# Kernel tuning notes

Hardware: AMD Instinct MI355X
Metric: run time of the kernel (lower is better)

Reference implementation:

```python
import jax, jax.numpy as jnp
import numpy as np

D_MODEL = 1024
D = 256
B, T = 64, 512


def setup_inputs() -> dict:
    key = jax.random.key(0)
    ks = jax.random.split(key, 7)
    s = 1.0 / np.sqrt(D_MODEL)
    return {
        "x": jax.random.normal(ks[0], (B, T, D_MODEL), dtype=jnp.float32),
        "Wq": jax.random.uniform(ks[1], (D_MODEL, D), jnp.float32, -s, s),
        "bq": jax.random.uniform(ks[2], (D,), jnp.float32, -s, s),
        "Wk": jax.random.uniform(ks[3], (D_MODEL, D), jnp.float32, -s, s),
        "bk": jax.random.uniform(ks[4], (D,), jnp.float32, -s, s),
        "Wv": jax.random.uniform(ks[5], (D_MODEL, D), jnp.float32, -s, s),
        "bv": jax.random.uniform(ks[6], (D,), jnp.float32, -s, s),
    }


def reference(x, Wq, bq, Wk, bk, Wv, bv):
    # Linear projections: [B,T,d_model] -> [B,T,d]
    q = x @ Wq + bq
    k = x @ Wk + bk
    v = x @ Wv + bv
    Tq = x.shape[1]
    scale = k.shape[-1] ** (-0.5)
    # scores: [B,T,T]
    scores = jnp.einsum('bqd,bkd->bqk', q, k) * scale
    causal = jnp.tril(jnp.ones((Tq, Tq), dtype=bool))
    scores = jnp.where(causal, scores, -jnp.inf)
    weights = jax.nn.softmax(scores, axis=-1)
    out = jnp.einsum('bqk,bkd->bqd', weights, v)
    return out
```

## Files before the change

### kernel.cpp

```cpp
#include <hip/hip_runtime.h>
#include <hip/hip_bf16.h>

typedef __attribute__((ext_vector_type(8))) short short8;
typedef __attribute__((ext_vector_type(4))) float floatx4;
typedef __attribute__((ext_vector_type(16))) float floatx16;

#define GLOAD_LDS16(src, dst) \
  __builtin_amdgcn_global_load_lds((const __attribute__((address_space(1))) unsigned int*)(src), \
      (__attribute__((address_space(3))) unsigned int*)(dst), 16, 0, 0)

__device__ __forceinline__ short f2bf(float f) {
    __hip_bfloat16 h = __float2bfloat16(f);
    return *reinterpret_cast<short*>(&h);
}

__device__ __forceinline__ floatx4 mfma16(short8 a, short8 b, floatx4 c) {
    return __builtin_amdgcn_mfma_f32_16x16x32_bf16(a, b, c, 0, 0, 0);
}

__device__ __forceinline__ floatx16 mfma32(short8 a, short8 b, floatx16 c) {
    return __builtin_amdgcn_mfma_f32_32x32x16_bf16(a, b, c, 0, 0, 0);
}

__global__ __launch_bounds__(256) void wconv_kernel(const float* __restrict__ Wq,
                                                    const float* __restrict__ Wk,
                                                    const float* __restrict__ Wv,
                                                    __hip_bfloat16* __restrict__ WT) {
    int n = blockIdx.x;
    const float* W = (n < 256) ? Wq : (n < 512 ? Wk : Wv);
    int nl = n & 255;
    __hip_bfloat16* dst = WT + (size_t)n * 1024;
    for (int kk = threadIdx.x; kk < 1024; kk += 256)
        dst[kk] = __float2bfloat16(W[(size_t)kk * 256 + nl]);
}

__global__ __launch_bounds__(512) void proj_kernel(const float* __restrict__ x,
                                                   const __hip_bfloat16* __restrict__ WT,
                                                   const float* __restrict__ bq,
                                                   const float* __restrict__ bk,
                                                   const float* __restrict__ bv,
                                                   __hip_bfloat16* __restrict__ qo,
                                                   __hip_bfloat16* __restrict__ ko,
                                                   __hip_bfloat16* __restrict__ vo) {
    __shared__ __align__(16) float As[128 * 64];
    __shared__ __align__(16) __hip_bfloat16 Bs[768 * 64];
    char* AsB = (char*)As;
    char* BsB = (char*)Bs;

    const int tid = threadIdx.x;
    const int m0 = blockIdx.x * 128;
    const int wid = tid >> 6, lane = tid & 63;
    const int wm = wid >> 2, wn = wid & 3;
    const int l31 = lane & 31, lh = lane >> 5;

    floatx16 acc[2][6];
#pragma unroll
    for (int i = 0; i < 2; ++i)
#pragma unroll
        for (int j = 0; j < 6; ++j)
#pragma unroll
            for (int e = 0; e < 16; ++e) acc[i][j][e] = 0.f;

    for (int kt = 0; kt < 16; ++kt) {
#pragma unroll
        for (int s = 0; s < 4; ++s) {
            int o = s * 8192 + tid * 16;
            int row = o >> 8;
            int sb = (o & 255) ^ ((row & 7) << 4);
            const float* src = x + (size_t)(m0 + row) * 1024 + kt * 64 + (sb >> 2);
            GLOAD_LDS16(src, AsB + o);
        }
#pragma unroll
        for (int s = 0; s < 12; ++s) {
            int o = s * 8192 + tid * 16;
            int row = o >> 7;
            int so = (o & 127) ^ ((row & 7) << 4);
            const __hip_bfloat16* src = WT + (size_t)row * 1024 + kt * 64 + (so >> 1);
            GLOAD_LDS16(src, BsB + o);
        }
        __syncthreads();

#pragma unroll
        for (int ks = 0; ks < 4; ++ks) {
            short8 af[2];
#pragma unroll
            for (int mt = 0; mt < 2; ++mt) {
                int row = wm * 64 + mt * 32 + l31;
                int rb = row * 256, msk = (row & 7) << 4;
                int b0 = ks * 64 + lh * 32;
                floatx4 f0 = *(const floatx4*)(AsB + rb + (b0 ^ msk));
                floatx4 f1 = *(const floatx4*)(AsB + rb + ((b0 + 16) ^ msk));
                short8 h;
                h[0] = f2bf(f0[0]); h[1] = f2bf(f0[1]); h[2] = f2bf(f0[2]); h[3] = f2bf(f0[3]);
                h[4] = f2bf(f1[0]); h[5] = f2bf(f1[1]); h[6] = f2bf(f1[2]); h[7] = f2bf(f1[3]);
                af[mt] = h;
            }
#pragma unroll
            for (int nt = 0; nt < 6; ++nt) {
                int row = wn * 192 + nt * 32 + l31;
                int off = ks * 32 + lh * 16;
                short8 b8 = *(const short8*)(BsB + row * 128 + (off ^ ((row & 7) << 4)));
                acc[0][nt] = mfma32(af[0], b8, acc[0][nt]);
                acc[1][nt] = mfma32(af[1], b8, acc[1][nt]);
            }
        }
        __syncthreads();
    }

#pragma unroll
    for (int nt = 0; nt < 6; ++nt) {
        int g = wn * 192 + nt * 32 + l31;
        int mat = g >> 8;
        const float* bias = (mat == 0) ? bq : (mat == 1 ? bk : bv);
        __hip_bfloat16* ob = (mat == 0) ? qo : (mat == 1 ? ko : vo);
        float scale = (mat == 0) ? 0.09016844005556021f : 1.0f;
        int c = g & 255;
        float bval = bias[c];
#pragma unroll
        for (int mt = 0; mt < 2; ++mt) {
            int base_row = m0 + wm * 64 + mt * 32 + lh * 4;
#pragma unroll
            for (int reg = 0; reg < 16; ++reg) {
                int row = base_row + (reg & 3) + 8 * (reg >> 2);
                ob[(size_t)row * 256 + c] = __float2bfloat16((acc[mt][nt][reg] + bval) * scale);
            }
        }
    }
}

__global__ __launch_bounds__(256) void attn_kernel(const __hip_bfloat16* __restrict__ q,
                                                   const __hip_bfloat16* __restrict__ k,
                                                   const __hip_bfloat16* __restrict__ v,
                                                   float* __restrict__ out) {
    __shared__ __align__(16) __hip_bfloat16 Ks[64 * 256];
    __shared__ __align__(16) __hip_bfloat16 VTs[256 * 64];
    __shared__ __align__(16) __hip_bfloat16 Ps[4][16 * 64];
    char* KsB = (char*)Ks;
    char* VTB = (char*)VTs;

    const int tid = threadIdx.x;
    const int bid = blockIdx.x;
    const int wgid = (bid & 7) * 64 + (bid >> 3);
    const int qb = wgid & 7, b = wgid >> 3;
    const int wid = tid >> 6, lane = tid & 63;
    const int l15 = lane & 15, lg = lane >> 4;
    char* PsB = (char*)(&Ps[wid][0]);

    short8 qf[8];
    const __hip_bfloat16* qrow = q + ((size_t)(b * 512 + qb * 64 + wid * 16 + l15)) * 256;
#pragma unroll
    for (int ks = 0; ks < 8; ++ks) qf[ks] = *(const short8*)(qrow + ks * 32 + lg * 8);

    float m_[4], lsum[4];
    floatx4 o[16];
#pragma unroll
    for (int r = 0; r < 4; ++r) { m_[r] = -1e30f; lsum[r] = 0.f; }
#pragma unroll
    for (int dt = 0; dt < 16; ++dt) o[dt] = (floatx4){0.f, 0.f, 0.f, 0.f};

    const int vkv = lane;
    const int vd0 = wid * 8;

    for (int c = 0; c <= qb; ++c) {
        const size_t kvbase = (size_t)(b * 512 + c * 64) * 256;
#pragma unroll
        for (int s = 0; s < 8; ++s) {
            int o_ = s * 4096 + tid * 16;
            int row = o_ >> 9;
            int so = o_ ^ ((row & 7) << 4);
            const __hip_bfloat16* src = k + kvbase + (size_t)row * 256 + ((so & 511) >> 1);
            GLOAD_LDS16(src, KsB + o_);
        }
#pragma unroll
        for (int it = 0; it < 8; ++it) {
            int dbase = vd0 + it * 32;
            short8 vv = *(const short8*)(v + kvbase + (size_t)vkv * 256 + dbase);
#pragma unroll
            for (int j = 0; j < 8; ++j) {
                int d = dbase + j;
                int addr = (d * 128 + vkv * 2) ^ ((d & 7) << 4);
                *(short*)(VTB + addr) = vv[j];
            }
        }
        __syncthreads();

        floatx4 s4[4];
#pragma unroll
        for (int t = 0; t < 4; ++t) s4[t] = (floatx4){0.f, 0.f, 0.f, 0.f};
#pragma unroll
        for (int ks = 0; ks < 8; ++ks) {
#pragma unroll
            for (int t = 0; t < 4; ++t) {
                int kv = t * 16 + l15;
                short8 kf = *(const short8*)(KsB + kv * 512 + ((ks * 64 + lg * 16) ^ ((kv & 7) << 4)));
                s4[t] = mfma16(qf[ks], kf, s4[t]);
            }
        }
        if (c == qb) {
#pragma unroll
            for (int t = 0; t < 4; ++t) {
                int kvl = t * 16 + l15;
#pragma unroll
                for (int r = 0; r < 4; ++r)
                    if (kvl > wid * 16 + lg * 4 + r) s4[t][r] = -1e30f;
            }
        }
        float pm[4], alpha[4], rs[4];
#pragma unroll
        for (int r = 0; r < 4; ++r)
            pm[r] = fmaxf(fmaxf(s4[0][r], s4[1][r]), fmaxf(s4[2][r], s4[3][r]));
#pragma unroll
        for (int off = 1; off <= 8; off <<= 1)
#pragma unroll
            for (int r = 0; r < 4; ++r) pm[r] = fmaxf(pm[r], __shfl_xor(pm[r], off));
#pragma unroll
        for (int r = 0; r < 4; ++r) {
            float mn = fmaxf(m_[r], pm[r]);
            alpha[r] = exp2f(m_[r] - mn);
            m_[r] = mn;
        }
#pragma unroll
        for (int t = 0; t < 4; ++t)
#pragma unroll
            for (int r = 0; r < 4; ++r) s4[t][r] = exp2f(s4[t][r] - m_[r]);
#pragma unroll
        for (int r = 0; r < 4; ++r) rs[r] = s4[0][r] + s4[1][r] + s4[2][r] + s4[3][r];
#pragma unroll
        for (int off = 1; off <= 8; off <<= 1)
#pragma unroll
            for (int r = 0; r < 4; ++r) rs[r] += __shfl_xor(rs[r], off);
#pragma unroll
        for (int r = 0; r < 4; ++r) lsum[r] = lsum[r] * alpha[r] + rs[r];
#pragma unroll
        for (int dt = 0; dt < 16; ++dt) {
            o[dt][0] *= alpha[0]; o[dt][1] *= alpha[1];
            o[dt][2] *= alpha[2]; o[dt][3] *= alpha[3];
        }
#pragma unroll
        for (int t = 0; t < 4; ++t)
#pragma unroll
            for (int r = 0; r < 4; ++r) {
                int qq = lg * 4 + r;
                int addr = (qq * 128 + (t * 16 + l15) * 2) ^ ((qq & 7) << 4);
                *(short*)(PsB + addr) = f2bf(s4[t][r]);
            }
#pragma unroll
        for (int h = 0; h < 2; ++h) {
            short8 pa = *(const short8*)(PsB + l15 * 128 + ((h * 64 + lg * 16) ^ ((l15 & 7) << 4)));
#pragma unroll
            for (int dt = 0; dt < 16; ++dt) {
                int d = dt * 16 + l15;
                short8 vb = *(const short8*)(VTB + d * 128 + ((h * 64 + lg * 16) ^ ((d & 7) << 4)));
                o[dt] = mfma16(pa, vb, o[dt]);
            }
        }
        __syncthreads();
    }

    float inv[4];
#pragma unroll
    for (int r = 0; r < 4; ++r) inv[r] = 1.0f / lsum[r];
    size_t obase = ((size_t)(b * 512 + qb * 64 + wid * 16 + lg * 4)) * 256 + l15;
#pragma unroll
    for (int dt = 0; dt < 16; ++dt)
#pragma unroll
        for (int r = 0; r < 4; ++r)
            out[obase + (size_t)r * 256 + dt * 16] = o[dt][r] * inv[r];
}

extern "C" void kernel_launch(void* const* d_in, const int* in_sizes, int n_in,
                              void* d_out, int out_size, void* d_ws, size_t ws_size,
                              hipStream_t stream) {
    const float* x  = (const float*)d_in[0];
    const float* Wq = (const float*)d_in[1];
    const float* bq = (const float*)d_in[2];
    const float* Wk = (const float*)d_in[3];
    const float* bk = (const float*)d_in[4];
    const float* Wv = (const float*)d_in[5];
    const float* bv = (const float*)d_in[6];
    float* out = (float*)d_out;

    char* ws = (char*)d_ws;
    __hip_bfloat16* WT = (__hip_bfloat16*)ws;
    __hip_bfloat16* qo = (__hip_bfloat16*)(ws + (2u << 20));
    __hip_bfloat16* ko = qo + (size_t)32768 * 256;
    __hip_bfloat16* vo = ko + (size_t)32768 * 256;

    wconv_kernel<<<dim3(768), dim3(256), 0, stream>>>(Wq, Wk, Wv, WT);
    proj_kernel<<<dim3(256), dim3(512), 0, stream>>>(x, WT, bq, bk, bv, qo, ko, vo);
    attn_kernel<<<dim3(512), dim3(256), 0, stream>>>(qo, ko, vo, out);
}
```

Before: 155.0 us.

## Double-buffer projection GEMM loads and tile the weight transpose through LDS

The projection GEMM now uses two LDS buffers with a K-step of 32, so async global-to-LDS loads for step kt+2 are issued while step kt is being computed. It uses vmcnt waits, raw barriers and MFMA priority hints in place of the old load-sync-compute loop. The weight transpose kernel is rewritten to transpose 64x64 tiles through padded shared memory, which gives coalesced reads and writes. The prefetch past the last step is clamped to a redundant reload of step 31, and the hand-set vmcnt count has to match the number of loads issued per stage.

Measured after the change: 159.1 us. 2.6% more time.

```diff
diff --git a/kernel.cpp b/kernel.cpp
--- a/kernel.cpp
+++ b/kernel.cpp
@@ -26,12 +26,29 @@
                                                     const float* __restrict__ Wk,
                                                     const float* __restrict__ Wv,
                                                     __hip_bfloat16* __restrict__ WT) {
-    int n = blockIdx.x;
-    const float* W = (n < 256) ? Wq : (n < 512 ? Wk : Wv);
-    int nl = n & 255;
-    __hip_bfloat16* dst = WT + (size_t)n * 1024;
-    for (int kk = threadIdx.x; kk < 1024; kk += 256)
-        dst[kk] = __float2bfloat16(W[(size_t)kk * 256 + nl]);
+    __shared__ unsigned short lds[64][65];
+    const int bidx = blockIdx.x;
+    const int kt = bidx & 15;
+    const int ntile = bidx >> 4;
+    const int gn0 = ntile * 64;
+    const float* W = (gn0 < 256) ? Wq : (gn0 < 512 ? Wk : Wv);
+    const int nl0 = gn0 & 255;
+    const int k0 = kt * 64;
+    const int tr = threadIdx.x >> 6;
+    const int tc = threadIdx.x & 63;
+
+#pragma unroll
+    for (int it = 0; it < 16; ++it) {
+        int r = it * 4 + tr;
+        lds[r][tc] = (unsigned short)f2bf(W[(size_t)(k0 + r) * 256 + nl0 + tc]);
+    }
+    __syncthreads();
+#pragma unroll
+    for (int it = 0; it < 16; ++it) {
+        int nr = it * 4 + tr;
+        unsigned short u = lds[tc][nr];
+        WT[(size_t)(gn0 + nr) * 1024 + k0 + tc] = *reinterpret_cast<__hip_bfloat16*>(&u);
+    }
 }
 
 __global__ __launch_bounds__(512) void proj_kernel(const float* __restrict__ x,
@@ -42,10 +59,8 @@
                                                    __hip_bfloat16* __restrict__ qo,
                                                    __hip_bfloat16* __restrict__ ko,
                                                    __hip_bfloat16* __restrict__ vo) {
-    __shared__ __align__(16) float As[128 * 64];
-    __shared__ __align__(16) __hip_bfloat16 Bs[768 * 64];
-    char* AsB = (char*)As;
-    char* BsB = (char*)Bs;
+    __shared__ __align__(16) char Ab[2][16384];
+    __shared__ __align__(16) char Bb[2][49152];
 
     const int tid = threadIdx.x;
     const int m0 = blockIdx.x * 128;
@@ -61,51 +76,70 @@
 #pragma unroll
             for (int e = 0; e < 16; ++e) acc[i][j][e] = 0.f;
 
-    for (int kt = 0; kt < 16; ++kt) {
-#pragma unroll
-        for (int s = 0; s < 4; ++s) {
-            int o = s * 8192 + tid * 16;
-            int row = o >> 8;
-            int sb = (o & 255) ^ ((row & 7) << 4);
-            const float* src = x + (size_t)(m0 + row) * 1024 + kt * 64 + (sb >> 2);
-            GLOAD_LDS16(src, AsB + o);
-        }
-#pragma unroll
-        for (int s = 0; s < 12; ++s) {
-            int o = s * 8192 + tid * 16;
-            int row = o >> 7;
-            int so = (o & 127) ^ ((row & 7) << 4);
-            const __hip_bfloat16* src = WT + (size_t)row * 1024 + kt * 64 + (so >> 1);
-            GLOAD_LDS16(src, BsB + o);
-        }
-        __syncthreads();
-
-#pragma unroll
-        for (int ks = 0; ks < 4; ++ks) {
+#define STAGE(KT, BUFI) do {                                                         \
+        _Pragma("unroll")                                                            \
+        for (int s = 0; s < 2; ++s) {                                                \
+            int o = s * 8192 + tid * 16;                                             \
+            int row = o >> 7;                                \
+            int sb = (o & 127) ^ ((row & 7) << 4);                                   \
+            const float* src = x + (size_t)(m0 + row) * 1024 + (KT) * 32 + (sb >> 2);\
+            GLOAD_LDS16(src, Ab[BUFI] + o);                                          \
+        }                                                                            \
+        _Pragma("unroll")                                                            \
+        for (int s = 0; s < 6; ++s) {                                                \
+            int o = s * 8192 + tid * 16;                                             \
+            int row = o >> 6;                                 \
+            int so = (o & 63) ^ ((row & 3) << 4);                                    \
+            const __hip_bfloat16* src = WT + (size_t)row * 1024 + (KT) * 32          \
+                                        + (so >> 1);                                 \
+            GLOAD_LDS16(src, Bb[BUFI] + o);                                          \
+        } } while (0)
+
+    STAGE(0, 0);
+    STAGE(1, 1);
+
+    for (int kt = 0; kt < 32; ++kt) {
+        const int cur = kt & 1;
+        __builtin_amdgcn_sched_barrier(0);
+        asm volatile("s_waitcnt vmcnt(8)" ::: "memory");
+        __builtin_amdgcn_sched_barrier(0);
+        __builtin_amdgcn_s_barrier();
+        __builtin_amdgcn_sched_barrier(0);
+
+#pragma unroll
+        for (int ks = 0; ks < 2; ++ks) {
             short8 af[2];
 #pragma unroll
             for (int mt = 0; mt < 2; ++mt) {
                 int row = wm * 64 + mt * 32 + l31;
-                int rb = row * 256, msk = (row & 7) << 4;
+                int rb = row * 128, msk = (row & 7) << 4;
                 int b0 = ks * 64 + lh * 32;
-                floatx4 f0 = *(const floatx4*)(AsB + rb + (b0 ^ msk));
-                floatx4 f1 = *(const floatx4*)(AsB + rb + ((b0 + 16) ^ msk));
+                floatx4 f0 = *(const floatx4*)(Ab[cur] + rb + (b0 ^ msk));
+                floatx4 f1 = *(const floatx4*)(Ab[cur] + rb + ((b0 + 16) ^ msk));
                 short8 h;
                 h[0] = f2bf(f0[0]); h[1] = f2bf(f0[1]); h[2] = f2bf(f0[2]); h[3] = f2bf(f0[3]);
                 h[4] = f2bf(f1[0]); h[5] = f2bf(f1[1]); h[6] = f2bf(f1[2]); h[7] = f2bf(f1[3]);
                 af[mt] = h;
             }
+            __builtin_amdgcn_s_setprio(1);
 #pragma unroll
             for (int nt = 0; nt < 6; ++nt) {
                 int row = wn * 192 + nt * 32 + l31;
                 int off = ks * 32 + lh * 16;
-                short8 b8 = *(const short8*)(BsB + row * 128 + (off ^ ((row & 7) << 4)));
+                short8 b8 = *(const short8*)(Bb[cur] + row * 64 + (off ^ ((row & 3) << 4)));
                 acc[0][nt] = mfma32(af[0], b8, acc[0][nt]);
                 acc[1][nt] = mfma32(af[1], b8, acc[1][nt]);
             }
-        }
-        __syncthreads();
-    }
+            __builtin_amdgcn_s_setprio(0);
+        }
+
+        __builtin_amdgcn_sched_barrier(0);
+        __builtin_amdgcn_s_barrier();
+        __builtin_amdgcn_sched_barrier(0);
+        int nxt = (kt + 2 > 31) ? 31 : kt + 2;
+        STAGE(nxt, cur);
+    }
+#undef STAGE
 
 #pragma unroll
     for (int nt = 0; nt < 6; ++nt) {
@@ -286,7 +320,7 @@
     __hip_bfloat16* ko = qo + (size_t)32768 * 256;
     __hip_bfloat16* vo = ko + (size_t)32768 * 256;
 
-    wconv_kernel<<<dim3(768), dim3(256), 0, stream>>>(Wq, Wk, Wv, WT);
+    wconv_kernel<<<dim3(192), dim3(256), 0, stream>>>(Wq, Wk, Wv, WT);
     proj_kernel<<<dim3(256), dim3(512), 0, stream>>>(x, WT, bq, bk, bv, qo, ko, vo);
     attn_kernel<<<dim3(512), dim3(256), 0, stream>>>(qo, ko, vo, out);
 }
```

## Pre-swizzle weights into MFMA fragment layout and load B directly from global

Applied to the files above, without the earlier changes.

The weight conversion kernel now writes bf16 weights in a layout where each 64-lane MFMA B-fragment is a contiguous 1 KB block. The projection kernel then loads B operands straight from global/L2 into registers instead of staging a 768x64 tile through LDS. This frees most of the shared memory, so the block shrinks to 64 rows and 4 waves and the grid doubles. The cost is that every block re-reads the full weight matrix from cache without LDS reuse across waves, and the global loads sit on the MFMA critical path with no explicit prefetch.

Result: slower. 294.4 us (+89.9%).

```diff
diff --git a/kernel.cpp b/kernel.cpp
--- a/kernel.cpp
+++ b/kernel.cpp
@@ -22,36 +22,44 @@
     return __builtin_amdgcn_mfma_f32_32x32x16_bf16(a, b, c, 0, 0, 0);
 }
 
-__global__ __launch_bounds__(256) void wconv_kernel(const float* __restrict__ Wq,
-                                                    const float* __restrict__ Wk,
-                                                    const float* __restrict__ Wv,
-                                                    __hip_bfloat16* __restrict__ WT) {
-    int n = blockIdx.x;
+__global__ __launch_bounds__(64) void wconv_kernel(const float* __restrict__ Wq,
+                                                   const float* __restrict__ Wk,
+                                                   const float* __restrict__ Wv,
+                                                   __hip_bfloat16* __restrict__ WTf) {
+    const int bid = blockIdx.x;
+    const int kb = bid / 24;
+    const int cb = bid % 24;
+    const int lane = threadIdx.x;
+    const int l31 = lane & 31, lh = lane >> 5;
+    const int n = cb * 32 + l31;
     const float* W = (n < 256) ? Wq : (n < 512 ? Wk : Wv);
-    int nl = n & 255;
-    __hip_bfloat16* dst = WT + (size_t)n * 1024;
-    for (int kk = threadIdx.x; kk < 1024; kk += 256)
-        dst[kk] = __float2bfloat16(W[(size_t)kk * 256 + nl]);
-}
-
-__global__ __launch_bounds__(512) void proj_kernel(const float* __restrict__ x,
-                                                   const __hip_bfloat16* __restrict__ WT,
+    const int nl = n & 255;
+    const int k0 = kb * 16 + lh * 8;
+
+    short8 h;
+#pragma unroll
+    for (int j = 0; j < 8; ++j)
+        h[j] = f2bf(W[(size_t)(k0 + j) * 256 + nl]);
+    *(short8*)((char*)WTf + (size_t)bid * 1024 + lane * 16) = h;
+}
+
+__global__ __launch_bounds__(256) void proj_kernel(const float* __restrict__ x,
+                                                   const __hip_bfloat16* __restrict__ WTf,
                                                    const float* __restrict__ bq,
                                                    const float* __restrict__ bk,
                                                    const float* __restrict__ bv,
                                                    __hip_bfloat16* __restrict__ qo,
                                                    __hip_bfloat16* __restrict__ ko,
                                                    __hip_bfloat16* __restrict__ vo) {
-    __shared__ __align__(16) float As[128 * 64];
-    __shared__ __align__(16) __hip_bfloat16 Bs[768 * 64];
+    __shared__ __align__(16) float As[64 * 64];
     char* AsB = (char*)As;
-    char* BsB = (char*)Bs;
 
     const int tid = threadIdx.x;
-    const int m0 = blockIdx.x * 128;
-    const int wid = tid >> 6, lane = tid & 63;
-    const int wm = wid >> 2, wn = wid & 3;
+    const int m0 = blockIdx.x * 64;
+    const int wn = tid >> 6;
+    const int lane = tid & 63;
     const int l31 = lane & 31, lh = lane >> 5;
+    const char* WTfB = (const char*)WTf;
 
     floatx16 acc[2][6];
 #pragma unroll
@@ -64,28 +72,27 @@
     for (int kt = 0; kt < 16; ++kt) {
 #pragma unroll
         for (int s = 0; s < 4; ++s) {
-            int o = s * 8192 + tid * 16;
+            int o = s * 4096 + tid * 16;
             int row = o >> 8;
             int sb = (o & 255) ^ ((row & 7) << 4);
             const float* src = x + (size_t)(m0 + row) * 1024 + kt * 64 + (sb >> 2);
             GLOAD_LDS16(src, AsB + o);
         }
-#pragma unroll
-        for (int s = 0; s < 12; ++s) {
-            int o = s * 8192 + tid * 16;
-            int row = o >> 7;
-            int so = (o & 127) ^ ((row & 7) << 4);
-            const __hip_bfloat16* src = WT + (size_t)row * 1024 + kt * 64 + (so >> 1);
-            GLOAD_LDS16(src, BsB + o);
-        }
         __syncthreads();
 
 #pragma unroll
         for (int ks = 0; ks < 4; ++ks) {
+            const int kb = kt * 4 + ks;
+            short8 b8[6];
+#pragma unroll
+            for (int nt = 0; nt < 6; ++nt) {
+                int cb = wn * 6 + nt;
+                b8[nt] = *(const short8*)(WTfB + ((size_t)(kb * 24 + cb) << 10) + lane * 16);
+            }
             short8 af[2];
 #pragma unroll
             for (int mt = 0; mt < 2; ++mt) {
-                int row = wm * 64 + mt * 32 + l31;
+                int row = mt * 32 + l31;
                 int rb = row * 256, msk = (row & 7) << 4;
                 int b0 = ks * 64 + lh * 32;
                 floatx4 f0 = *(const floatx4*)(AsB + rb + (b0 ^ msk));
@@ -97,11 +104,8 @@
             }
 #pragma unroll
             for (int nt = 0; nt < 6; ++nt) {
-                int row = wn * 192 + nt * 32 + l31;
-                int off = ks * 32 + lh * 16;
-                short8 b8 = *(const short8*)(BsB + row * 128 + (off ^ ((row & 7) << 4)));
-                acc[0][nt] = mfma32(af[0], b8, acc[0][nt]);
-                acc[1][nt] = mfma32(af[1], b8, acc[1][nt]);
+                acc[0][nt] = mfma32(af[0], b8[nt], acc[0][nt]);
+                acc[1][nt] = mfma32(af[1], b8[nt], acc[1][nt]);
             }
         }
         __syncthreads();
@@ -118,7 +122,7 @@
         float bval = bias[c];
 #pragma unroll
         for (int mt = 0; mt < 2; ++mt) {
-            int base_row = m0 + wm * 64 + mt * 32 + lh * 4;
+            int base_row = m0 + mt * 32 + lh * 4;
 #pragma unroll
             for (int reg = 0; reg < 16; ++reg) {
                 int row = base_row + (reg & 3) + 8 * (reg >> 2);
@@ -281,12 +285,12 @@
     float* out = (float*)d_out;
 
     char* ws = (char*)d_ws;
-    __hip_bfloat16* WT = (__hip_bfloat16*)ws;
+    __hip_bfloat16* WTf = (__hip_bfloat16*)ws;
     __hip_bfloat16* qo = (__hip_bfloat16*)(ws + (2u << 20));
     __hip_bfloat16* ko = qo + (size_t)32768 * 256;
     __hip_bfloat16* vo = ko + (size_t)32768 * 256;
 
-    wconv_kernel<<<dim3(768), dim3(256), 0, stream>>>(Wq, Wk, Wv, WT);
-    proj_kernel<<<dim3(256), dim3(512), 0, stream>>>(x, WT, bq, bk, bv, qo, ko, vo);
+    wconv_kernel<<<dim3(1536), dim3(64), 0, stream>>>(Wq, Wk, Wv, WTf);
+    proj_kernel<<<dim3(512), dim3(256), 0, stream>>>(x, WTf, bq, bk, bv, qo, ko, vo);
     attn_kernel<<<dim3(512), dim3(256), 0, stream>>>(qo, ko, vo, out);
 }
```
